# Kernel optimization log

Hardware: AMD Instinct MI355X
Metric: run time of the kernel (lower is better)

## Reference

```python
import jax, jax.numpy as jnp
import numpy as np

SEQ, D_IN, D_OUT = 8192, 768, 64


def setup_inputs() -> dict:
    key = jax.random.key(0)
    k0, k1, k2, k3 = jax.random.split(key, 4)
    x = jax.random.normal(k0, (SEQ, D_IN), dtype=jnp.float32)
    # nn.Linear default init ~ U(-1/sqrt(d_in), 1/sqrt(d_in)); small scale keeps softmax stable
    s = 0.02
    Wq = jax.random.normal(k1, (D_IN, D_OUT), dtype=jnp.float32) * s
    Wk = jax.random.normal(k2, (D_IN, D_OUT), dtype=jnp.float32) * s
    Wv = jax.random.normal(k3, (D_IN, D_OUT), dtype=jnp.float32) * s
    return {"x": x, "Wq": Wq, "Wk": Wk, "Wv": Wv}


def reference(x, Wq, Wk, Wv):
    # queries/keys/values: [S, d_out]
    q = x @ Wq
    k = x @ Wk
    v = x @ Wv
    d_k = k.shape[-1]
    scores = q @ k.T / jnp.sqrt(jnp.asarray(d_k, x.dtype))  # [S, S]
    weights = jax.nn.softmax(scores, axis=-1)
    return weights @ v  # [S, d_out]
```

## Files before the change

kernel.cpp:

```cpp
#include <hip/hip_runtime.h>
#include <hip/hip_bf16.h>

#define SEQ  8192
#define DIN  768
#define DOUT 64

typedef __attribute__((ext_vector_type(8))) short short8;
typedef __attribute__((ext_vector_type(4))) short s16x4;
typedef __attribute__((ext_vector_type(4))) float f32x4;

__device__ inline unsigned short f2bf(float f) {
    __hip_bfloat16 h = __float2bfloat16(f);
    return __builtin_bit_cast(unsigned short, h);
}

__global__ __launch_bounds__(256) void wconv_kernel(
    const float* __restrict__ Wq, const float* __restrict__ Wk,
    const float* __restrict__ Wv, unsigned short* __restrict__ Wf) {
    int idx = blockIdx.x * 256 + threadIdx.x;
    int c = idx / DIN;
    int k = idx - c * DIN;
    int sel = c >> 6, cc = c & 63;
    const float* W = (sel == 0) ? Wq : ((sel == 1) ? Wk : Wv);
    float v = W[k * DOUT + cc];
    if (sel == 0) v *= 0.125f * 1.4426950408889634f;
    int nt = c >> 4, l15 = c & 15;
    int kt = k >> 6, k6 = k & 63;
    int h  = k6 >> 5, r5 = k6 & 31, g = r5 >> 3, e = r5 & 7;
    Wf[(((kt * 12 + nt) * 2 + h) << 9) + (g << 7) + (l15 << 3) + e] = f2bf(v);
}

__global__ __launch_bounds__(256) void proj_kernel(
    const float* __restrict__ x, const unsigned short* __restrict__ Wf,
    unsigned short* __restrict__ Q8, unsigned short* __restrict__ Kf,
    unsigned short* __restrict__ Vf) {
    __shared__ unsigned short xs[2][16 * 136];

    const int tid  = threadIdx.x;
    const int m0   = blockIdx.x * 16;
    const int lane = tid & 63;
    const int w    = tid >> 6;
    const int g    = lane >> 4;
    const int l15  = lane & 15;
    const int sr   = tid >> 4;
    const int sc8  = (tid & 15) * 8;

    f32x4 zero = {0.f, 0.f, 0.f, 0.f};
    f32x4 acc[3] = {zero, zero, zero};

    auto stage = [&](int kk, int buf) {
        const float4* s4 = reinterpret_cast<const float4*>(
            &x[(m0 + sr) * DIN + kk * 128 + sc8]);
        float4 f0 = s4[0], f1 = s4[1];
        short8 o8;
        o8[0]=(short)f2bf(f0.x); o8[1]=(short)f2bf(f0.y); o8[2]=(short)f2bf(f0.z); o8[3]=(short)f2bf(f0.w);
        o8[4]=(short)f2bf(f1.x); o8[5]=(short)f2bf(f1.y); o8[6]=(short)f2bf(f1.z); o8[7]=(short)f2bf(f1.w);
        *(short8*)&xs[buf][sr * 136 + sc8] = o8;
    };

    stage(0, 0);
    __syncthreads();

    for (int kk = 0; kk < 6; ++kk) {
        const int buf = kk & 1;
        short8 a00 = *(short8*)&xs[buf][l15 * 136 + g * 8];
        short8 a01 = *(short8*)&xs[buf][l15 * 136 + g * 8 + 32];
        short8 a10 = *(short8*)&xs[buf][l15 * 136 + g * 8 + 64];
        short8 a11 = *(short8*)&xs[buf][l15 * 136 + g * 8 + 96];
        if (kk + 1 < 6) stage(kk + 1, buf ^ 1);
#pragma unroll
        for (int i = 0; i < 3; ++i) {
            int nt  = w * 3 + i;
            int kt0 = 2 * kk, kt1 = 2 * kk + 1;
            const unsigned short* wb0 = &Wf[((kt0 * 12 + nt) * 2) * 512 + lane * 8];
            const unsigned short* wb1 = &Wf[((kt1 * 12 + nt) * 2) * 512 + lane * 8];
            acc[i] = __builtin_amdgcn_mfma_f32_16x16x32_bf16(a00, *(const short8*)wb0,         acc[i], 0, 0, 0);
            acc[i] = __builtin_amdgcn_mfma_f32_16x16x32_bf16(a01, *(const short8*)(wb0 + 512), acc[i], 0, 0, 0);
            acc[i] = __builtin_amdgcn_mfma_f32_16x16x32_bf16(a10, *(const short8*)wb1,         acc[i], 0, 0, 0);
            acc[i] = __builtin_amdgcn_mfma_f32_16x16x32_bf16(a11, *(const short8*)(wb1 + 512), acc[i], 0, 0, 0);
        }
        __syncthreads();
    }
#pragma unroll
    for (int i = 0; i < 3; ++i) {
#pragma unroll
        for (int r = 0; r < 4; ++r) {
            int row = m0 + g * 4 + r;
            int col = (w * 3 + i) * 16 + l15;
            unsigned short b = f2bf(acc[i][r]);
            if (col < 64) {
                Q8[row * 64 + col] = b;
            } else if (col < 128) {
                int d  = col - 64;
                int t  = row >> 6, nt = (row >> 4) & 3, lk = row & 15;
                int h  = d >> 5, kg = (d >> 3) & 3, e = d & 7;
                Kf[(((t * 4 + nt) * 2 + h) * 64 + kg * 16 + lk) * 8 + e] = b;
            } else {
                int d  = col - 128;
                int kv = row;
                int t  = kv >> 6, k6 = kv & 63;
                int c  = k6 >> 5, r5 = k6 & 31;
                int hf = r5 >> 4, vg = (r5 >> 2) & 3, j = (r5 & 3) + hf * 4;
                int dn = d >> 4, lv = d & 15;
                Vf[(((t * 2 + c) * 4 + dn) * 64 + vg * 16 + lv) * 8 + j] = b;
            }
        }
    }
}

__global__ __launch_bounds__(256, 2) void flash_kernel(
    const unsigned short* __restrict__ Q8, const unsigned short* __restrict__ Kf,
    const unsigned short* __restrict__ Vf, float* __restrict__ Op,
    float* __restrict__ Lp, int ntiles) {
    const int tid  = threadIdx.x;
    const int w    = tid >> 6;
    const int lane = tid & 63;
    const int g    = lane >> 4;
    const int l15  = lane & 15;
    const int q0   = (blockIdx.x * 4 + w) * 64;
    const int nsub = ntiles * 2;
    const int sub0 = blockIdx.y * nsub;

    short8 qa[8];
#pragma unroll
    for (int qg = 0; qg < 4; ++qg) {
        qa[qg * 2 + 0] = *(const short8*)&Q8[(q0 + qg * 16 + l15) * 64 + g * 8];
        qa[qg * 2 + 1] = *(const short8*)&Q8[(q0 + qg * 16 + l15) * 64 + g * 8 + 32];
    }

    short8 onesf;
#pragma unroll
    for (int j = 0; j < 8; ++j) onesf[j] = (short)0x3F80;

    f32x4 zero = {0.f, 0.f, 0.f, 0.f};
    f32x4 o[4][4];
    f32x4 oL[4] = {zero, zero, zero, zero};
#pragma unroll
    for (int qg = 0; qg < 4; ++qg)
#pragma unroll
        for (int dn = 0; dn < 4; ++dn) o[qg][dn] = zero;

    const unsigned short* kfp = Kf + (size_t)sub0 * 2048 + lane * 8;
    const unsigned short* vfp = Vf + (size_t)sub0 * 2048 + lane * 8;

    short8 kb[2][2], vA[4], vB[4];
#pragma unroll
    for (int nt = 0; nt < 2; ++nt)
#pragma unroll
        for (int h = 0; h < 2; ++h)
            kb[nt][h] = *(const short8*)&kfp[(nt * 2 + h) * 512];
#pragma unroll
    for (int dn = 0; dn < 4; ++dn)
        vA[dn] = *(const short8*)&vfp[dn * 512];

#define FLASH_STEP(I, VCUR, VNXT)                                                            \
    {                                                                                        \
        f32x4 s[4][2];                                                                       \
        _Pragma("unroll")                                                                    \
        for (int qg = 0; qg < 4; ++qg)                                                       \
            _Pragma("unroll")                                                                \
            for (int nt = 0; nt < 2; ++nt) s[qg][nt] = zero;                                 \
        __builtin_amdgcn_s_setprio(1);                                                       \
        _Pragma("unroll")                                                                    \
        for (int nt = 0; nt < 2; ++nt)                                                       \
            _Pragma("unroll")                                                                \
            for (int qg = 0; qg < 4; ++qg) {                                                 \
                s[qg][nt] = __builtin_amdgcn_mfma_f32_16x16x32_bf16(kb[nt][0], qa[qg * 2 + 0], s[qg][nt], 0, 0, 0); \
                s[qg][nt] = __builtin_amdgcn_mfma_f32_16x16x32_bf16(kb[nt][1], qa[qg * 2 + 1], s[qg][nt], 0, 0, 0); \
            }                                                                                \
        __builtin_amdgcn_s_setprio(0);                                                       \
        if ((I) + 1 < nsub) {                                                                \
            _Pragma("unroll")                                                                \
            for (int nt = 0; nt < 2; ++nt)                                                   \
                _Pragma("unroll")                                                            \
                for (int h = 0; h < 2; ++h)                                                  \
                    kb[nt][h] = *(const short8*)&kfp[(size_t)((I) + 1) * 2048 + (nt * 2 + h) * 512]; \
            _Pragma("unroll")                                                                \
            for (int dn = 0; dn < 4; ++dn)                                                   \
                VNXT[dn] = *(const short8*)&vfp[(size_t)((I) + 1) * 2048 + dn * 512];        \
        }                                                                                    \
        short8 pa[4];                                                                        \
        _Pragma("unroll")                                                                    \
        for (int qg = 0; qg < 4; ++qg) {                                                     \
            float p[8];                                                                      \
            _Pragma("unroll")                                                                \
            for (int nt = 0; nt < 2; ++nt)                                                   \
                _Pragma("unroll")                                                            \
                for (int r = 0; r < 4; ++r)                                                  \
                    p[nt * 4 + r] = __builtin_amdgcn_exp2f(s[qg][nt][r]);                    \
            short8 pk;                                                                       \
            _Pragma("unroll")                                                                \
            for (int j = 0; j < 8; ++j) pk[j] = (short)f2bf(p[j]);                           \
            pa[qg] = pk;                                                                     \
        }                                                                                    \
        __builtin_amdgcn_s_setprio(1);                                                       \
        _Pragma("unroll")                                                                    \
        for (int qg = 0; qg < 4; ++qg)                                                       \
            oL[qg] = __builtin_amdgcn_mfma_f32_16x16x32_bf16(onesf, pa[qg], oL[qg], 0, 0, 0); \
        _Pragma("unroll")                                                                    \
        for (int dn = 0; dn < 4; ++dn)                                                       \
            _Pragma("unroll")                                                                \
            for (int qg = 0; qg < 4; ++qg)                                                   \
                o[qg][dn] = __builtin_amdgcn_mfma_f32_16x16x32_bf16(VCUR[dn], pa[qg], o[qg][dn], 0, 0, 0); \
        __builtin_amdgcn_s_setprio(0);                                                       \
    }

    for (int i = 0; i < nsub; i += 2) {
        FLASH_STEP(i, vA, vB)
        FLASH_STEP(i + 1, vB, vA)
    }
#undef FLASH_STEP

    const size_t sb = (size_t)blockIdx.y * SEQ;
#pragma unroll
    for (int qg = 0; qg < 4; ++qg) {
#pragma unroll
        for (int dn = 0; dn < 4; ++dn)
            *(f32x4*)&Op[(sb + q0 + qg * 16 + l15) * 64 + dn * 16 + 4 * g] = o[qg][dn];
        if (g == 0) {
            Lp[sb + q0 + qg * 16 + l15] = oL[qg][0];
        }
    }
}

__global__ __launch_bounds__(256) void reduce_kernel(
    const float* __restrict__ Op, const float* __restrict__ Lp,
    float* __restrict__ Out, int NS) {
    int q  = blockIdx.x * 16 + (threadIdx.x >> 4);
    int d4 = (threadIdx.x & 15) * 4;
    float L = 0.f;
    f32x4 acc = {0.f, 0.f, 0.f, 0.f};
    for (int s = 0; s < NS; ++s) {
        L   += Lp[s * SEQ + q];
        acc += *(const f32x4*)&Op[((size_t)s * SEQ + q) * 64 + d4];
    }
    float inv = 1.0f / L;
    f32x4 r = {acc[0] * inv, acc[1] * inv, acc[2] * inv, acc[3] * inv};
    *(f32x4*)&Out[q * 64 + d4] = r;
}

extern "C" void kernel_launch(void* const* d_in, const int* in_sizes, int n_in,
                              void* d_out, int out_size, void* d_ws, size_t ws_size,
                              hipStream_t stream) {
    const float* x  = (const float*)d_in[0];
    const float* Wq = (const float*)d_in[1];
    const float* Wk = (const float*)d_in[2];
    const float* Wv = (const float*)d_in[3];
    float* out = (float*)d_out;

    char* ws = (char*)d_ws;
    unsigned short* Wf = (unsigned short*)(ws);
    unsigned short* Q8 = (unsigned short*)(ws + 294912);
    unsigned short* Kf = (unsigned short*)(ws + 294912 + 1048576);
    unsigned short* Vf = (unsigned short*)(ws + 294912 + 2097152);
    const size_t fixed = 294912 + 3 * 1048576;

    int NS = 16;
    while (NS > 1 && fixed + (size_t)NS * (2097152 + 32768) > ws_size) NS >>= 1;
    float* Op = (float*)(ws + fixed);
    float* Lp = (float*)(ws + fixed + (size_t)NS * 2097152);
    const int ntiles = SEQ / (NS * 64);

    wconv_kernel<<<dim3(576), dim3(256), 0, stream>>>(Wq, Wk, Wv, Wf);
    proj_kernel<<<dim3(512), dim3(256), 0, stream>>>(x, Wf, Q8, Kf, Vf);
    flash_kernel<<<dim3(32, NS), dim3(256), 0, stream>>>(Q8, Kf, Vf, Op, Lp, ntiles);
    reduce_kernel<<<dim3(512), dim3(256), 0, stream>>>(Op, Lp, out, NS);
}
```

Measured before the change: 49.34 us.

## Fuse split-K reduction into flash kernel via last-block atomic ticket

Removes the separate reduce kernel launch. Each flash block bumps a per-query-tile atomic counter after writing its partial output, and the last block for that tile sums all split partials and writes the normalized result. Counters are zeroed in the weight-conversion kernel. This saves a launch and the gap between kernels, but the reduction is serialized onto 32 trailing blocks with one query row per thread and strided loads.

```diff
diff --git a/kernel.cpp b/kernel.cpp
--- a/kernel.cpp
+++ b/kernel.cpp
@@ -16,7 +16,9 @@
 
 __global__ __launch_bounds__(256) void wconv_kernel(
     const float* __restrict__ Wq, const float* __restrict__ Wk,
-    const float* __restrict__ Wv, unsigned short* __restrict__ Wf) {
+    const float* __restrict__ Wv, unsigned short* __restrict__ Wf,
+    int* __restrict__ Cnt) {
+    if (blockIdx.x == 0 && threadIdx.x < 64) Cnt[threadIdx.x] = 0;
     int idx = blockIdx.x * 256 + threadIdx.x;
     int c = idx / DIN;
     int k = idx - c * DIN;
@@ -111,7 +113,9 @@
 __global__ __launch_bounds__(256, 2) void flash_kernel(
     const unsigned short* __restrict__ Q8, const unsigned short* __restrict__ Kf,
     const unsigned short* __restrict__ Vf, float* __restrict__ Op,
-    float* __restrict__ Lp, int ntiles) {
+    float* __restrict__ Lp, float* __restrict__ Outp, int* __restrict__ Cnt,
+    int ntiles) {
+    __shared__ int ticket_s;
     const int tid  = threadIdx.x;
     const int w    = tid >> 6;
     const int lane = tid & 63;
@@ -221,22 +225,38 @@
             Lp[sb + q0 + qg * 16 + l15] = oL[qg][0];
         }
     }
-}
-
-__global__ __launch_bounds__(256) void reduce_kernel(
-    const float* __restrict__ Op, const float* __restrict__ Lp,
-    float* __restrict__ Out, int NS) {
-    int q  = blockIdx.x * 16 + (threadIdx.x >> 4);
-    int d4 = (threadIdx.x & 15) * 4;
-    float L = 0.f;
-    f32x4 acc = {0.f, 0.f, 0.f, 0.f};
-    for (int s = 0; s < NS; ++s) {
-        L   += Lp[s * SEQ + q];
-        acc += *(const f32x4*)&Op[((size_t)s * SEQ + q) * 64 + d4];
-    }
-    float inv = 1.0f / L;
-    f32x4 r = {acc[0] * inv, acc[1] * inv, acc[2] * inv, acc[3] * inv};
-    *(f32x4*)&Out[q * 64 + d4] = r;
+
+    __threadfence();
+    if (tid == 0) ticket_s = atomicAdd(&Cnt[blockIdx.x], 1);
+    __syncthreads();
+    if (ticket_s == (int)gridDim.y - 1) {
+        __threadfence();
+        const int NS = gridDim.y;
+        const int q  = blockIdx.x * 256 + tid;
+        float L = 0.f;
+        for (int s = 0; s < NS; ++s) L += Lp[(size_t)s * SEQ + q];
+        float inv = 1.0f / L;
+#pragma unroll
+        for (int c = 0; c < 4; ++c) {
+            f32x4 a0 = zero, a1 = zero, a2 = zero, a3 = zero;
+            for (int s = 0; s < NS; ++s) {
+                const float* bp = &Op[((size_t)s * SEQ + q) * 64 + c * 16];
+                a0 += *(const f32x4*)(bp + 0);
+                a1 += *(const f32x4*)(bp + 4);
+                a2 += *(const f32x4*)(bp + 8);
+                a3 += *(const f32x4*)(bp + 12);
+            }
+            float* ob = &Outp[(size_t)q * 64 + c * 16];
+            f32x4 r0 = {a0[0]*inv, a0[1]*inv, a0[2]*inv, a0[3]*inv};
+            f32x4 r1 = {a1[0]*inv, a1[1]*inv, a1[2]*inv, a1[3]*inv};
+            f32x4 r2 = {a2[0]*inv, a2[1]*inv, a2[2]*inv, a2[3]*inv};
+            f32x4 r3 = {a3[0]*inv, a3[1]*inv, a3[2]*inv, a3[3]*inv};
+            *(f32x4*)(ob + 0)  = r0;
+            *(f32x4*)(ob + 4)  = r1;
+            *(f32x4*)(ob + 8)  = r2;
+            *(f32x4*)(ob + 12) = r3;
+        }
+    }
 }
 
 extern "C" void kernel_launch(void* const* d_in, const int* in_sizes, int n_in,
@@ -256,13 +276,13 @@
     const size_t fixed = 294912 + 3 * 1048576;
 
     int NS = 16;
-    while (NS > 1 && fixed + (size_t)NS * (2097152 + 32768) > ws_size) NS >>= 1;
+    while (NS > 1 && fixed + (size_t)NS * (2097152 + 32768) + 256 > ws_size) NS >>= 1;
     float* Op = (float*)(ws + fixed);
     float* Lp = (float*)(ws + fixed + (size_t)NS * 2097152);
+    int*   Cnt = (int*)(ws + fixed + (size_t)NS * 2097152 + (size_t)NS * 32768);
     const int ntiles = SEQ / (NS * 64);
 
-    wconv_kernel<<<dim3(576), dim3(256), 0, stream>>>(Wq, Wk, Wv, Wf);
+    wconv_kernel<<<dim3(576), dim3(256), 0, stream>>>(Wq, Wk, Wv, Wf, Cnt);
     proj_kernel<<<dim3(512), dim3(256), 0, stream>>>(x, Wf, Q8, Kf, Vf);
-    flash_kernel<<<dim3(32, NS), dim3(256), 0, stream>>>(Q8, Kf, Vf, Op, Lp, ntiles);
-    reduce_kernel<<<dim3(512), dim3(256), 0, stream>>>(Op, Lp, out, NS);
-}
+    flash_kernel<<<dim3(32, NS), dim3(256), 0, stream>>>(Q8, Kf, Vf, Op, Lp, out, Cnt, ntiles);
+}
```

After: 146.7 us. +197.3%, slower.
